# Optimization experiments

Measured on AMD Instinct MI355X. Metric: run time of the kernel, lower is better.

Reference implementation:

```python
import jax, jax.numpy as jnp
import numpy as np

B, S, D, H, W = 2, 2048, 1024, 16, 16  # batch, seq, embed, heads, window
HD = D // H
DFF = 4 * D
EPS = 1e-5


def _ln(x, g, b):
    m = jnp.mean(x, axis=-1, keepdims=True)
    v = jnp.mean(jnp.square(x - m), axis=-1, keepdims=True)
    return (x - m) * jax.lax.rsqrt(v + EPS) * g + b


def setup_inputs() -> dict:
    key = jax.random.key(0)
    ks = jax.random.split(key, 12)
    s = 0.02
    return {
        "x": jax.random.normal(ks[0], (B, S, D), jnp.float32),
        "ln1_g": jnp.ones((D,), jnp.float32),
        "ln1_b": jnp.zeros((D,), jnp.float32),
        "in_proj_w": jax.random.normal(ks[1], (3 * D, D), jnp.float32) * s,
        "in_proj_b": jnp.zeros((3 * D,), jnp.float32),
        "out_proj_w": jax.random.normal(ks[2], (D, D), jnp.float32) * s,
        "out_proj_b": jnp.zeros((D,), jnp.float32),
        "ln2_g": jnp.ones((D,), jnp.float32),
        "ln2_b": jnp.zeros((D,), jnp.float32),
        "mlp_w1": jax.random.normal(ks[3], (DFF, D), jnp.float32) * s,
        "mlp_b1": jnp.zeros((DFF,), jnp.float32),
        "mlp_w2": jax.random.normal(ks[4], (D, DFF), jnp.float32) * s,
        "mlp_b2": jnp.zeros((D,), jnp.float32),
    }


def reference(x, ln1_g, ln1_b, in_proj_w, in_proj_b, out_proj_w, out_proj_b,
              ln2_g, ln2_b, mlp_w1, mlp_b1, mlp_w2, mlp_b2):
    h = _ln(x, ln1_g, ln1_b)
    qkv = h @ in_proj_w.T + in_proj_b  # [B,S,3D]
    q, k, v = jnp.split(qkv, 3, axis=-1)
    q = q.reshape(B, S, H, HD)
    k = k.reshape(B, S, H, HD)
    v = v.reshape(B, S, H, HD)
    scores = jnp.einsum("bqhd,bkhd->bhqk", q, k) / jnp.sqrt(jnp.float32(HD))
    idx = jnp.arange(S)
    dlt = idx[:, None] - idx[None, :]
    allowed = (dlt >= 0) & (dlt < W)  # causal sliding window, width W
    scores = jnp.where(allowed, scores, -jnp.inf)
    attn = jax.nn.softmax(scores, axis=-1)
    o = jnp.einsum("bhqk,bkhd->bqhd", attn, v).reshape(B, S, D)
    o = o @ out_proj_w.T + out_proj_b
    x = x + o  # residual 1
    xn = _ln(x, ln2_g, ln2_b)
    mlp = jax.nn.gelu(xn @ mlp_w1.T + mlp_b1) @ mlp_w2.T + mlp_b2
    return x + mlp
```

## Files before the change

### kernel.cpp

```cpp
#include <hip/hip_runtime.h>
#include <hip/hip_bf16.h>
#include <cmath>

typedef __bf16 bf16;
typedef __bf16 bf16x4 __attribute__((ext_vector_type(4)));
typedef __bf16 bf16x8 __attribute__((ext_vector_type(8)));
typedef float f32x4 __attribute__((ext_vector_type(4)));

#define BB 2
#define SS 2048
#define DD 1024
#define HH 16
#define WW 16
#define HDD 64
#define DFFD 4096
#define NTOK (BB*SS)

__device__ __forceinline__ float gelu_f(float x) {
    const float k = 1.5957691216057308f;
    float u = k * (x + 0.044715f * x * x * x);
    return x / (1.0f + __expf(-u));
}

__device__ __forceinline__ void glds16(const bf16* g, const bf16* l) {
    __builtin_amdgcn_global_load_lds(
        (const __attribute__((address_space(1))) void*)(uintptr_t)(const void*)g,
        (__attribute__((address_space(3))) void*)(unsigned)(uintptr_t)(const void*)l,
        16, 0, 0);
}

__global__ __launch_bounds__(256) void conv2_kernel(
    const float* __restrict__ s0, bf16* __restrict__ d0, int n0,
    const float* __restrict__ s1, bf16* __restrict__ d1, int n1)
{
    int i = blockIdx.x * 256 + threadIdx.x;
    const float* src; bf16* dst; int idx;
    if (i < n0) { src = s0; dst = d0; idx = i; }
    else        { idx = i - n0; if (idx >= n1) return; src = s1; dst = d1; }
    f32x4 a = *(const f32x4*)(src + (size_t)idx * 8);
    f32x4 b = *(const f32x4*)(src + (size_t)idx * 8 + 4);
    bf16x8 v;
#pragma unroll
    for (int j = 0; j < 4; j++) { v[j] = (bf16)a[j]; v[4 + j] = (bf16)b[j]; }
    *(bf16x8*)(dst + (size_t)idx * 8) = v;
}

__global__ __launch_bounds__(256) void ln_kernel(
    const float* __restrict__ x, const float* __restrict__ g, const float* __restrict__ b,
    bf16* __restrict__ out)
{
    const int row = blockIdx.x, t = threadIdx.x;
    f32x4 v = *(const f32x4*)(x + (size_t)row * DD + t * 4);
    float s  = v[0] + v[1] + v[2] + v[3];
    float s2 = v[0]*v[0] + v[1]*v[1] + v[2]*v[2] + v[3]*v[3];
#pragma unroll
    for (int off = 32; off >= 1; off >>= 1) {
        s  += __shfl_xor(s,  off, 64);
        s2 += __shfl_xor(s2, off, 64);
    }
    __shared__ float red[8];
    const int wave = t >> 6;
    if ((t & 63) == 0) { red[wave] = s; red[4 + wave] = s2; }
    __syncthreads();
    float ts  = red[0] + red[1] + red[2] + red[3];
    float ts2 = red[4] + red[5] + red[6] + red[7];
    float mean = ts * (1.0f / DD);
    float var  = ts2 * (1.0f / DD) - mean * mean;
    float rstd = rsqrtf(var + 1e-5f);
    f32x4 gv = *(const f32x4*)(g + t * 4);
    f32x4 bv = *(const f32x4*)(b + t * 4);
    bf16x4 o;
#pragma unroll
    for (int i = 0; i < 4; i++) o[i] = (bf16)((v[i] - mean) * rstd * gv[i] + bv[i]);
    *(bf16x4*)(out + (size_t)row * DD + t * 4) = o;
}

template<int TM, int ACT, int RESID, int OUTF32>
__global__ __launch_bounds__(256) void gemm_glds(
    const bf16* __restrict__ A, const bf16* __restrict__ Bw,
    const float* __restrict__ bias,
    const float* resid, void* __restrict__ Cout, int N, int K)
{
    constexpr int MI = 4;
    constexpr int NJ = (TM == 128) ? 4 : 2;
    __shared__ __align__(16) bf16 As[3 * TM * 32];
    __shared__ __align__(16) bf16 Bs[3 * 128 * 32];
    const int t = threadIdx.x;
    const int nbxy = gridDim.x * gridDim.y;
    const int bid  = blockIdx.y * gridDim.x + blockIdx.x;
    const int cpx  = nbxy >> 3;
    const int swz  = (bid & 7) * cpx + (bid >> 3);
    const int m0 = (swz / gridDim.x) * TM;
    const int n0 = (swz % gridDim.x) * 128;
    const int lane = t & 63, w = t >> 6;
    const int wm = (TM == 128) ? (w & 1) * 64 : 0;
    const int wn = (TM == 128) ? (w >> 1) * 64 : w * 32;
    const int quad = lane >> 4, l16 = lane & 15;
    const int srow = t >> 2;
    const int qsw  = (t & 3) ^ ((srow >> 1) & 3);

    const bf16* Ag = A  + (size_t)(m0 + srow) * K + qsw * 8;
    const bf16* Bg = Bw + (size_t)(n0 + srow) * K + qsw * 8;

    int k_lo = 0, k_hi = K;
    if (RESID == 3) {
        const int ks = K / gridDim.z;
        k_lo = blockIdx.z * ks;
        k_hi = k_lo + ks;
    }

    auto stage = [&](int buf, int k0) {
        const bf16* AsW = As + buf * (TM * 32) + w * 512;
        const bf16* BsW = Bs + buf * (128 * 32) + w * 512;
        glds16(Ag + k0, AsW);
        if (TM == 128) glds16(Ag + (size_t)64 * K + k0, AsW + 2048);
        glds16(Bg + k0, BsW);
        glds16(Bg + (size_t)64 * K + k0, BsW + 2048);
    };

    const f32x4 zero = {0.f, 0.f, 0.f, 0.f};
    f32x4 acc[MI][NJ];
#pragma unroll
    for (int i = 0; i < MI; i++)
#pragma unroll
        for (int j = 0; j < NJ; j++) acc[i][j] = zero;

    const int nsteps = (k_hi - k_lo) >> 5;
    stage(0, k_lo);
    if (nsteps > 1) stage(1, k_lo + 32);

    const int rsl = (quad ^ ((l16 >> 1) & 3)) * 8;
    int cur = 0, nxt2 = 2;
    for (int step = 0; step < nsteps; ++step) {
        if (step < nsteps - 1) {
            if (TM == 128) asm volatile("s_waitcnt vmcnt(4)" ::: "memory");
            else           asm volatile("s_waitcnt vmcnt(3)" ::: "memory");
        } else {
            asm volatile("s_waitcnt vmcnt(0)" ::: "memory");
        }
        __builtin_amdgcn_s_barrier();
        if (step + 2 < nsteps) stage(nxt2, k_lo + ((step + 2) << 5));
        const bf16* Ab = As + cur * (TM * 32);
        const bf16* Bb = Bs + cur * (128 * 32);
        bf16x8 af[MI], bfr[NJ];
#pragma unroll
        for (int i = 0; i < MI; i++)
            af[i] = *(const bf16x8*)(Ab + (wm + i * 16 + l16) * 32 + rsl);
#pragma unroll
        for (int j = 0; j < NJ; j++)
            bfr[j] = *(const bf16x8*)(Bb + (wn + j * 16 + l16) * 32 + rsl);
#pragma unroll
        for (int i = 0; i < MI; i++)
#pragma unroll
            for (int j = 0; j < NJ; j++)
                acc[i][j] = __builtin_amdgcn_mfma_f32_16x16x32_bf16(af[i], bfr[j], acc[i][j], 0, 0, 0);
        cur  = (cur  + 1 == 3) ? 0 : cur  + 1;
        nxt2 = (nxt2 + 1 == 3) ? 0 : nxt2 + 1;
    }

#pragma unroll
    for (int i = 0; i < MI; i++) {
#pragma unroll
        for (int j = 0; j < NJ; j++) {
            int col = n0 + wn + j * 16 + l16;
            float bv = bias[col];
            if (RESID == 3 && blockIdx.z != 0) bv = 0.0f;
#pragma unroll
            for (int r = 0; r < 4; r++) {
                int row = m0 + wm + i * 16 + quad * 4 + r;
                float val = acc[i][j][r] + bv;
                if (ACT == 1) val = gelu_f(val);
                size_t idx = (size_t)row * N + col;
                if (RESID == 2) val += resid[idx];
                if (RESID == 3) {
                    unsafeAtomicAdd(&((float*)Cout)[idx], val);
                } else if (OUTF32) {
                    ((float*)Cout)[idx] = val;
                } else {
                    ((bf16*)Cout)[idx] = (bf16)val;
                }
            }
        }
    }
}

__global__ __launch_bounds__(256) void attn_kernel(
    const bf16* __restrict__ qkv, bf16* __restrict__ o)
{
    __shared__ __align__(16) bf16 Vlds[4][32 * 64];
    __shared__ __align__(16) bf16 Plds[4][16 * 32];
    const int t = threadIdx.x;
    const int w = t >> 6, lane = t & 63;
    const int quad = lane >> 4, l16 = lane & 15;
    const int gw = blockIdx.x * 4 + w;
    const int qb = gw & 127;
    const int h  = (gw >> 7) & (HH - 1);
    const int b  = gw >> 11;
    const int q0 = qb << 4;
    const size_t rs = 3 * DD;
    const bf16* Qb = qkv + (size_t)b * SS * rs + h * HDD;
    const bf16* Kb = Qb + DD;
    const bf16* Vb = Qb + 2 * DD;
    bf16* Vw = Vlds[w];
    bf16* Pw = Plds[w];

    {
        const int sub = lane >> 3;
        const int dc  = (lane & 7) * 8;
#pragma unroll
        for (int c = 0; c < 4; c++) {
            int key = q0 - 16 + c * 8 + sub;
            if (key < 0) key = 0;
            glds16(Vb + (size_t)key * rs + dc, Vw + c * 512);
        }
    }

    const int qrow = q0 + l16;
    int kr0 = q0 - 16 + l16; if (kr0 < 0) kr0 = 0;
    bf16x8 qf0  = *(const bf16x8*)(Qb + (size_t)qrow * rs + quad * 8);
    bf16x8 qf1  = *(const bf16x8*)(Qb + (size_t)qrow * rs + 32 + quad * 8);
    bf16x8 kf0a = *(const bf16x8*)(Kb + (size_t)kr0  * rs + quad * 8);
    bf16x8 kf0b = *(const bf16x8*)(Kb + (size_t)kr0  * rs + 32 + quad * 8);
    bf16x8 kf1a = *(const bf16x8*)(Kb + (size_t)qrow * rs + quad * 8);
    bf16x8 kf1b = *(const bf16x8*)(Kb + (size_t)qrow * rs + 32 + quad * 8);

    const f32x4 zero = {0.f, 0.f, 0.f, 0.f};
    f32x4 acc0 = __builtin_amdgcn_mfma_f32_16x16x32_bf16(qf0, kf0a, zero, 0, 0, 0);
    acc0 = __builtin_amdgcn_mfma_f32_16x16x32_bf16(qf1, kf0b, acc0, 0, 0, 0);
    f32x4 acc1 = __builtin_amdgcn_mfma_f32_16x16x32_bf16(qf0, kf1a, zero, 0, 0, 0);
    acc1 = __builtin_amdgcn_mfma_f32_16x16x32_bf16(qf1, kf1b, acc1, 0, 0, 0);

    float rl[4];
#pragma unroll
    for (int r = 0; r < 4; r++) {
        const int row = quad * 4 + r;
        float s0 = (l16 > row && q0 - 16 + l16 >= 0) ? acc0[r] * 0.125f : -1e30f;
        float s1 = (l16 <= row)                      ? acc1[r] * 0.125f : -1e30f;
        float m = fmaxf(s0, s1);
        m = fmaxf(m, __shfl_xor(m, 1, 64));
        m = fmaxf(m, __shfl_xor(m, 2, 64));
        m = fmaxf(m, __shfl_xor(m, 4, 64));
        m = fmaxf(m, __shfl_xor(m, 8, 64));
        float e0 = __expf(s0 - m), e1 = __expf(s1 - m);
        float sum = e0 + e1;
        sum += __shfl_xor(sum, 1, 64);
        sum += __shfl_xor(sum, 2, 64);
        sum += __shfl_xor(sum, 4, 64);
        sum += __shfl_xor(sum, 8, 64);
        rl[r] = 1.0f / sum;
        Pw[row * 32 + l16]      = (bf16)e0;
        Pw[row * 32 + 16 + l16] = (bf16)e1;
    }

    asm volatile("s_waitcnt vmcnt(0)" ::: "memory");
    bf16x8 pf = *(const bf16x8*)(Pw + l16 * 32 + quad * 8);
#pragma unroll
    for (int dt = 0; dt < 4; dt++) {
        bf16x8 vf;
#pragma unroll
        for (int jj = 0; jj < 8; jj++)
            vf[jj] = Vw[(quad * 8 + jj) * 64 + dt * 16 + l16];
        f32x4 ov = __builtin_amdgcn_mfma_f32_16x16x32_bf16(pf, vf, zero, 0, 0, 0);
#pragma unroll
        for (int r = 0; r < 4; r++) {
            const int row = quad * 4 + r;
            o[(size_t)(b * SS + q0 + row) * DD + h * HDD + dt * 16 + l16] =
                (bf16)(ov[r] * rl[r]);
        }
    }
}

extern "C" void kernel_launch(void* const* d_in, const int* in_sizes, int n_in,
                              void* d_out, int out_size, void* d_ws, size_t ws_size,
                              hipStream_t stream)
{
    (void)in_sizes; (void)n_in; (void)out_size; (void)ws_size;
    const float* x    = (const float*)d_in[0];
    const float* ln1g = (const float*)d_in[1];
    const float* ln1b = (const float*)d_in[2];
    const float* Wqkv = (const float*)d_in[3];
    const float* bqkv = (const float*)d_in[4];
    const float* Wout = (const float*)d_in[5];
    const float* bout = (const float*)d_in[6];
    const float* ln2g = (const float*)d_in[7];
    const float* ln2b = (const float*)d_in[8];
    const float* W1   = (const float*)d_in[9];
    const float* b1   = (const float*)d_in[10];
    const float* W2   = (const float*)d_in[11];
    const float* b2   = (const float*)d_in[12];

    const size_t MB = (size_t)1 << 20;
    char* ws = (char*)d_ws;
    bf16* wqkv_bf = (bf16*)(ws);
    bf16* wout_bf = (bf16*)(ws + 6 * MB);
    bf16* w1_bf   = (bf16*)(ws);
    bf16* w2_bf   = (bf16*)(ws + 8 * MB);
    bf16* qkv     = (bf16*)(ws + 16 * MB);
    bf16* h1      = (bf16*)(ws + 16 * MB);
    bf16* hbuf    = (bf16*)(ws + 48 * MB);
    float* x1     = (float*)d_out;

    const dim3 blk(256);

    {
        const int n0 = 3 * DD * DD / 8, n1 = DD * DD / 8;
        conv2_kernel<<<(n0 + n1 + 255) / 256, blk, 0, stream>>>(
            Wqkv, wqkv_bf, n0, Wout, wout_bf, n1);
    }
    ln_kernel<<<NTOK, blk, 0, stream>>>(x, ln1g, ln1b, hbuf);
    gemm_glds<128, 0, 0, 0><<<dim3(24, 32), blk, 0, stream>>>(
        hbuf, wqkv_bf, bqkv, nullptr, qkv, 3 * DD, DD);
    attn_kernel<<<BB * HH * (SS / 16) / 4, blk, 0, stream>>>(qkv, hbuf);
    gemm_glds<64, 0, 2, 1><<<dim3(8, 64), blk, 0, stream>>>(
        hbuf, wout_bf, bout, x, x1, DD, DD);

    {
        const int n0 = DFFD * DD / 8, n1 = DFFD * DD / 8;
        conv2_kernel<<<(n0 + n1 + 255) / 256, blk, 0, stream>>>(
            W1, w1_bf, n0, W2, w2_bf, n1);
    }
    ln_kernel<<<NTOK, blk, 0, stream>>>(x1, ln2g, ln2b, hbuf);
    gemm_glds<128, 1, 0, 0><<<dim3(32, 32), blk, 0, stream>>>(
        hbuf, w1_bf, b1, nullptr, h1, DFFD, DD);
    gemm_glds<128, 0, 3, 1><<<dim3(8, 32, 2), blk, 0, stream>>>(
        h1, w2_bf, b2, nullptr, x1, DD, DFFD);
}
```

Baseline: 299.4 us.

## Deepen GEMM LDS pipeline to four stages and fuse weight conversion with layernorm

The GEMM kernel now keeps four LDS buffers and prefetches three k-steps ahead instead of two, with adjusted vmcnt waits, so more global loads are in flight. The weight fp32→bf16 conversion and layernorm launches are merged into one kernel whose first blocks convert weights and remaining blocks do layernorm rows. This removes two launches and lets the two independent jobs overlap. The larger LDS footprint may reduce blocks per CU.

Result: no change. 298.4 us (-0.3%).

```diff
diff --git a/kernel.cpp b/kernel.cpp
--- a/kernel.cpp
+++ b/kernel.cpp
@@ -29,28 +29,28 @@
         16, 0, 0);
 }
 
-__global__ __launch_bounds__(256) void conv2_kernel(
+__global__ __launch_bounds__(256) void conv2ln_kernel(
     const float* __restrict__ s0, bf16* __restrict__ d0, int n0,
-    const float* __restrict__ s1, bf16* __restrict__ d1, int n1)
+    const float* __restrict__ s1, bf16* __restrict__ d1, int n1, int ncb,
+    const float* __restrict__ xin, const float* __restrict__ g,
+    const float* __restrict__ b, bf16* __restrict__ lnout)
 {
-    int i = blockIdx.x * 256 + threadIdx.x;
-    const float* src; bf16* dst; int idx;
-    if (i < n0) { src = s0; dst = d0; idx = i; }
-    else        { idx = i - n0; if (idx >= n1) return; src = s1; dst = d1; }
-    f32x4 a = *(const f32x4*)(src + (size_t)idx * 8);
-    f32x4 b = *(const f32x4*)(src + (size_t)idx * 8 + 4);
-    bf16x8 v;
-#pragma unroll
-    for (int j = 0; j < 4; j++) { v[j] = (bf16)a[j]; v[4 + j] = (bf16)b[j]; }
-    *(bf16x8*)(dst + (size_t)idx * 8) = v;
-}
-
-__global__ __launch_bounds__(256) void ln_kernel(
-    const float* __restrict__ x, const float* __restrict__ g, const float* __restrict__ b,
-    bf16* __restrict__ out)
-{
-    const int row = blockIdx.x, t = threadIdx.x;
-    f32x4 v = *(const f32x4*)(x + (size_t)row * DD + t * 4);
+    const int t = threadIdx.x;
+    if ((int)blockIdx.x < ncb) {
+        int i = blockIdx.x * 256 + t;
+        const float* src; bf16* dst; int idx;
+        if (i < n0) { src = s0; dst = d0; idx = i; }
+        else        { idx = i - n0; if (idx >= n1) return; src = s1; dst = d1; }
+        f32x4 a = *(const f32x4*)(src + (size_t)idx * 8);
+        f32x4 c = *(const f32x4*)(src + (size_t)idx * 8 + 4);
+        bf16x8 v;
+#pragma unroll
+        for (int j = 0; j < 4; j++) { v[j] = (bf16)a[j]; v[4 + j] = (bf16)c[j]; }
+        *(bf16x8*)(dst + (size_t)idx * 8) = v;
+        return;
+    }
+    const int row = blockIdx.x - ncb;
+    f32x4 v = *(const f32x4*)(xin + (size_t)row * DD + t * 4);
     float s  = v[0] + v[1] + v[2] + v[3];
     float s2 = v[0]*v[0] + v[1]*v[1] + v[2]*v[2] + v[3]*v[3];
 #pragma unroll
@@ -72,7 +72,7 @@
     bf16x4 o;
 #pragma unroll
     for (int i = 0; i < 4; i++) o[i] = (bf16)((v[i] - mean) * rstd * gv[i] + bv[i]);
-    *(bf16x4*)(out + (size_t)row * DD + t * 4) = o;
+    *(bf16x4*)(lnout + (size_t)row * DD + t * 4) = o;
 }
 
 template<int TM, int ACT, int RESID, int OUTF32>
@@ -83,8 +83,8 @@
 {
     constexpr int MI = 4;
     constexpr int NJ = (TM == 128) ? 4 : 2;
-    __shared__ __align__(16) bf16 As[3 * TM * 32];
-    __shared__ __align__(16) bf16 Bs[3 * 128 * 32];
+    __shared__ __align__(16) bf16 As[4 * TM * 32];
+    __shared__ __align__(16) bf16 Bs[4 * 128 * 32];
     const int t = threadIdx.x;
     const int nbxy = gridDim.x * gridDim.y;
     const int bid  = blockIdx.y * gridDim.x + blockIdx.x;
@@ -128,20 +128,23 @@
     const int nsteps = (k_hi - k_lo) >> 5;
     stage(0, k_lo);
     if (nsteps > 1) stage(1, k_lo + 32);
+    if (nsteps > 2) stage(2, k_lo + 64);
 
     const int rsl = (quad ^ ((l16 >> 1) & 3)) * 8;
-    int cur = 0, nxt2 = 2;
     for (int step = 0; step < nsteps; ++step) {
-        if (step < nsteps - 1) {
+        if (step < nsteps - 2) {
+            if (TM == 128) asm volatile("s_waitcnt vmcnt(8)" ::: "memory");
+            else           asm volatile("s_waitcnt vmcnt(6)" ::: "memory");
+        } else if (step == nsteps - 2) {
             if (TM == 128) asm volatile("s_waitcnt vmcnt(4)" ::: "memory");
             else           asm volatile("s_waitcnt vmcnt(3)" ::: "memory");
         } else {
             asm volatile("s_waitcnt vmcnt(0)" ::: "memory");
         }
         __builtin_amdgcn_s_barrier();
-        if (step + 2 < nsteps) stage(nxt2, k_lo + ((step + 2) << 5));
-        const bf16* Ab = As + cur * (TM * 32);
-        const bf16* Bb = Bs + cur * (128 * 32);
+        if (step + 3 < nsteps) stage((step + 3) & 3, k_lo + ((step + 3) << 5));
+        const bf16* Ab = As + (step & 3) * (TM * 32);
+        const bf16* Bb = Bs + (step & 3) * (128 * 32);
         bf16x8 af[MI], bfr[NJ];
 #pragma unroll
         for (int i = 0; i < MI; i++)
@@ -154,8 +157,6 @@
 #pragma unroll
             for (int j = 0; j < NJ; j++)
                 acc[i][j] = __builtin_amdgcn_mfma_f32_16x16x32_bf16(af[i], bfr[j], acc[i][j], 0, 0, 0);
-        cur  = (cur  + 1 == 3) ? 0 : cur  + 1;
-        nxt2 = (nxt2 + 1 == 3) ? 0 : nxt2 + 1;
     }
 
 #pragma unroll
@@ -304,10 +305,10 @@
 
     {
         const int n0 = 3 * DD * DD / 8, n1 = DD * DD / 8;
-        conv2_kernel<<<(n0 + n1 + 255) / 256, blk, 0, stream>>>(
-            Wqkv, wqkv_bf, n0, Wout, wout_bf, n1);
-    }
-    ln_kernel<<<NTOK, blk, 0, stream>>>(x, ln1g, ln1b, hbuf);
+        const int ncb = (n0 + n1) / 256;
+        conv2ln_kernel<<<ncb + NTOK, blk, 0, stream>>>(
+            Wqkv, wqkv_bf, n0, Wout, wout_bf, n1, ncb, x, ln1g, ln1b, hbuf);
+    }
     gemm_glds<128, 0, 0, 0><<<dim3(24, 32), blk, 0, stream>>>(
         hbuf, wqkv_bf, bqkv, nullptr, qkv, 3 * DD, DD);
     attn_kernel<<<BB * HH * (SS / 16) / 4, blk, 0, stream>>>(qkv, hbuf);
@@ -316,10 +317,10 @@
 
     {
         const int n0 = DFFD * DD / 8, n1 = DFFD * DD / 8;
-        conv2_kernel<<<(n0 + n1 + 255) / 256, blk, 0, stream>>>(
-            W1, w1_bf, n0, W2, w2_bf, n1);
-    }
-    ln_kernel<<<NTOK, blk, 0, stream>>>(x1, ln2g, ln2b, hbuf);
+        const int ncb = (n0 + n1) / 256;
+        conv2ln_kernel<<<ncb + NTOK, blk, 0, stream>>>(
+            W1, w1_bf, n0, W2, w2_bf, n1, ncb, x1, ln2g, ln2b, hbuf);
+    }
     gemm_glds<128, 1, 0, 0><<<dim3(32, 32), blk, 0, stream>>>(
         hbuf, w1_bf, b1, nullptr, h1, DFFD, DD);
     gemm_glds<128, 0, 3, 1><<<dim3(8, 32, 2), blk, 0, stream>>>(
```
